# Optimization experiments

Hardware: AMD Instinct MI355X
Metric: run time of the kernel (lower is better)

Reference implementation:

```python
import jax, jax.numpy as jnp
import numpy as np

B, LQ, LK = 2, 2048, 77
DIM, XDIM = 320, 768
H, HD = 8, 40  # heads, head_dim; DIM == H*HD
FF = 4 * DIM  # GEGLU inner dim


def _ln(x, g, b, eps=1e-5):
    m = x.mean(-1, keepdims=True)
    v = ((x - m) ** 2).mean(-1, keepdims=True)
    return (x - m) * jax.lax.rsqrt(v + eps) * g + b


def _split_heads(x):  # [B,L,DIM] -> [B,H,L,HD]
    return x.reshape(x.shape[0], x.shape[1], H, HD).transpose(0, 2, 1, 3)


def _merge_heads(x):  # [B,H,L,HD] -> [B,L,DIM]
    return x.transpose(0, 2, 1, 3).reshape(x.shape[0], x.shape[2], H * HD)


def setup_inputs() -> dict:
    key = jax.random.key(0)
    ks = jax.random.split(key, 24)
    s = 0.02
    r = lambda i, shp: s * jax.random.normal(ks[i], shp, jnp.float32)
    return {
        "hidden_states": jax.random.normal(ks[0], (B, LQ, DIM), jnp.float32),
        "encoder_hidden_states": jax.random.normal(ks[1], (B, LK, XDIM), jnp.float32),
        # norm1 + self-attn (attn1)
        "ln1_g": jnp.ones((DIM,), jnp.float32), "ln1_b": jnp.zeros((DIM,), jnp.float32),
        "wq1": r(2, (DIM, DIM)), "wk1": r(3, (DIM, DIM)), "wv1": r(4, (DIM, DIM)),
        "wo1": r(5, (DIM, DIM)), "bo1": jnp.zeros((DIM,), jnp.float32),
        # norm2 + Hadamard cross-attn (attn2)
        "ln2_g": jnp.ones((DIM,), jnp.float32), "ln2_b": jnp.zeros((DIM,), jnp.float32),
        "wq2": r(6, (DIM, DIM)), "wk2": r(7, (XDIM, DIM)), "wvh": r(8, (DIM, DIM)),
        "wo2": r(9, (DIM, DIM)), "bo2": jnp.zeros((DIM,), jnp.float32),
        # norm3 + GEGLU feed-forward
        "ln3_g": jnp.ones((DIM,), jnp.float32), "ln3_b": jnp.zeros((DIM,), jnp.float32),
        "wff1": r(10, (DIM, 2 * FF)), "bff1": jnp.zeros((2 * FF,), jnp.float32),
        "wff2": r(11, (FF, DIM)), "bff2": jnp.zeros((DIM,), jnp.float32),
    }


def reference(hidden_states, encoder_hidden_states, ln1_g, ln1_b, wq1, wk1, wv1,
              wo1, bo1, ln2_g, ln2_b, wq2, wk2, wvh, wo2, bo2, ln3_g, ln3_b,
              wff1, bff1, wff2, bff2):
    scale = 1.0 / jnp.sqrt(jnp.asarray(HD, hidden_states.dtype))

    # ---- self-attention (SDPA semantics) ----
    h = _ln(hidden_states, ln1_g, ln1_b)
    q = _split_heads(h @ wq1)
    k = _split_heads(h @ wk1)
    v = _split_heads(h @ wv1)
    scores = jnp.einsum('bhqd,bhkd->bhqk', q, k) * scale
    w = jax.nn.softmax(scores, axis=-1)
    attn = jnp.einsum('bhqk,bhkd->bhqd', w, v)
    attn = _merge_heads(attn) @ wo1 + bo1
    hidden_states = hidden_states + attn

    # ---- Hadamard cross-attention: value comes from hidden_states (len Lq) ----
    h = _ln(hidden_states, ln2_g, ln2_b)
    q = _split_heads(h @ wq2)                     # [B,H,Lq,HD]
    k = _split_heads(encoder_hidden_states @ wk2) # [B,H,Lk,HD]
    vH = _split_heads(h @ wvh)                    # [B,H,Lq,HD]
    scores = jnp.einsum('bhqd,bhkd->bhqk', q, k) * scale
    w = jax.nn.softmax(scores, axis=-1)           # [B,H,Lq,Lk]
    # (w[...,None] * vH[...,None,:]).sum(-2) == vH * w.sum(-1, keepdims) (v indep of k)
    cross = vH * jnp.sum(w, axis=-1, keepdims=True)
    cross = _merge_heads(cross) @ wo2 + bo2
    hidden_states = hidden_states + cross

    # ---- GEGLU feed-forward ----
    h = _ln(hidden_states, ln3_g, ln3_b)
    proj = h @ wff1 + bff1
    x, gate = jnp.split(proj, 2, axis=-1)
    ff = (x * jax.nn.gelu(gate, approximate=False)) @ wff2 + bff2
    return hidden_states + ff
```

## Files before the change

kernel.cpp:

```cpp
#include <hip/hip_runtime.h>
#include <math.h>

#define DIM   320
#define HD    40
#define NH    8
#define LQ    2048
#define BATCH 2
#define MROWS 4096
#define FFD   1280
#define FF2   2560

#define KSPLIT 8
#define KCHUNK (LQ/KSPLIT)
#define KT     32
#define NT     (KCHUNK/KT)
#define NQROWS (BATCH*NH*LQ)

#define LSCALE (0.15811388300841897f * 1.4426950408889634f)

typedef unsigned short ushort_t;
typedef unsigned int u32;
using bf16x8 = __attribute__((ext_vector_type(8))) short;
using f32x4  = __attribute__((ext_vector_type(4))) float;

static __device__ inline ushort_t f2bf(float f) {
  union { float f; unsigned u; } x{f};
  unsigned r = x.u + 0x7FFFu + ((x.u >> 16) & 1u);
  return (ushort_t)(r >> 16);
}
static __device__ inline float bf2f(ushort_t h) {
  union { unsigned u; float f; } x; x.u = ((unsigned)h) << 16; return x.f;
}

__global__ __launch_bounds__(256) void ln_kernel(
    const float* __restrict__ X, const float* __restrict__ g,
    const float* __restrict__ bta, ushort_t* __restrict__ Y)
{
  int row  = blockIdx.x * 4 + (threadIdx.x >> 6);
  int lane = threadIdx.x & 63;
  const float* x = X + (size_t)row * DIM;
  float v[5];
  float s = 0.f;
#pragma unroll
  for (int i = 0; i < 5; ++i) { v[i] = x[lane + 64*i]; s += v[i]; }
#pragma unroll
  for (int off = 32; off >= 1; off >>= 1) s += __shfl_xor(s, off, 64);
  float mean = s * (1.0f/DIM);
  float sq = 0.f;
#pragma unroll
  for (int i = 0; i < 5; ++i) { float d = v[i] - mean; sq += d*d; }
#pragma unroll
  for (int off = 32; off >= 1; off >>= 1) sq += __shfl_xor(sq, off, 64);
  float rstd = rsqrtf(sq*(1.0f/DIM) + 1e-5f);
  ushort_t* y = Y + (size_t)row * DIM;
#pragma unroll
  for (int i = 0; i < 5; ++i) {
    int c = lane + 64*i;
    y[c] = f2bf((v[i]-mean)*rstd*g[c] + bta[c]);
  }
}

#define OFF_WQKVT 0
#define OFF_WO1T  (960*320)
#define OFF_WO2T  (OFF_WO1T + 320*320)
#define OFF_WFF1T (OFF_WO2T + 320*320)
#define OFF_WFF2T (OFF_WFF1T + 320*2560)
#define OFF_WVHB  (OFF_WFF2T + 1280*320)
#define WBF_TOTAL (OFF_WVHB + 320*320)

__global__ __launch_bounds__(256) void convw_kernel(
    const float* __restrict__ wq1, const float* __restrict__ wk1,
    const float* __restrict__ wv1, const float* __restrict__ wo1,
    const float* __restrict__ wo2, const float* __restrict__ wff1,
    const float* __restrict__ wff2, const float* __restrict__ wvh,
    ushort_t* __restrict__ dst, ushort_t* __restrict__ Kimg)
{
  int e = blockIdx.y;
  if (e == 8) {
    int f = blockIdx.x*256 + threadIdx.x;
    if (f < 98304) {
      int g3 = f/3, cidx = f - 3*g3;
      int rr = g3 & 31, tile = (g3 >> 5) & 63, bh = g3 >> 11;
      uint4 z = {0,0,0,0};
      *(uint4*)(Kimg + ((size_t)(bh*64 + tile))*2048 + rr*64
                + (((5+cidx) ^ (rr&7)) << 3)) = z;
    }
    return;
  }
  const float* src; int K, N; size_t doff; int tr = 1; float scale = 1.f;
  switch (e) {
    case 0: src=wq1;  K=320;  N=320;  doff=OFF_WQKVT; scale=LSCALE; break;
    case 1: src=wk1;  K=320;  N=320;  doff=OFF_WQKVT + 320*320;  break;
    case 2: src=wv1;  K=320;  N=320;  doff=OFF_WQKVT + 2*320*320;break;
    case 3: src=wo1;  K=320;  N=320;  doff=OFF_WO1T;             break;
    case 4: src=wo2;  K=320;  N=320;  doff=OFF_WO2T;             break;
    case 5: src=wff1; K=320;  N=2560; doff=OFF_WFF1T;            break;
    case 6: src=wff2; K=1280; N=320;  doff=OFF_WFF2T;            break;
    default: src=wvh; K=320;  N=320;  doff=OFF_WVHB; tr=0;       break;
  }
  int ntN = N/32;
  int nt_total = (K/32)*ntN;
  int t = blockIdx.x;
  if (t >= nt_total) return;
  int kt = t / ntN, nt = t - kt*ntN;
  __shared__ float tile[32][33];
  int tx = threadIdx.x & 31, ty = threadIdx.x >> 5;
  ushort_t* d = dst + doff;
#pragma unroll
  for (int i = 0; i < 4; ++i) {
    int r = ty + 8*i;
    tile[r][tx] = src[(size_t)(kt*32+r)*N + nt*32+tx] * scale;
  }
  __syncthreads();
  if (tr) {
#pragma unroll
    for (int i = 0; i < 4; ++i) {
      int r = ty + 8*i;
      d[(size_t)(nt*32+r)*K + kt*32+tx] = f2bf(tile[tx][r]);
    }
  } else {
#pragma unroll
    for (int i = 0; i < 4; ++i) {
      int r = ty + 8*i;
      d[(size_t)(kt*32+r)*N + nt*32+tx] = f2bf(tile[r][tx]);
    }
  }
}

#define AST 72
__global__ __launch_bounds__(256) void mgemm(
    const ushort_t* __restrict__ A, int lda,
    const ushort_t* __restrict__ Bt, int ldb,
    const float* __restrict__ bias,
    const float* __restrict__ R,
    float* __restrict__ Cf, ushort_t* __restrict__ Cb, int ldc,
    int K)
{
  __shared__ ushort_t As[64*AST];
  __shared__ ushort_t Bs[64*AST];
  int tid = threadIdx.x;
  int w = tid >> 6, lane = tid & 63, quad = lane >> 4, n16 = lane & 15;
  int wm = w >> 1, wn = w & 1;
  int bm = blockIdx.y * 64, bn = blockIdx.x * 64;
  int sr = tid >> 2, sc = (tid & 3) << 4;
  const ushort_t* Ag = A  + (size_t)(bm + sr)*lda + sc;
  const ushort_t* Bg = Bt + (size_t)(bn + sr)*ldb + sc;

  f32x4 acc00 = {0.f,0.f,0.f,0.f}, acc01 = acc00, acc10 = acc00, acc11 = acc00;

  float4 av0 = *(const float4*)(Ag);
  float4 av1 = *(const float4*)(Ag + 8);
  float4 bv0 = *(const float4*)(Bg);
  float4 bv1 = *(const float4*)(Bg + 8);
  for (int k0 = 0; k0 < K; k0 += 64) {
    __syncthreads();
    *(float4*)(As + sr*AST + sc)     = av0;
    *(float4*)(As + sr*AST + sc + 8) = av1;
    *(float4*)(Bs + sr*AST + sc)     = bv0;
    *(float4*)(Bs + sr*AST + sc + 8) = bv1;
    __syncthreads();
    if (k0 + 64 < K) {
      av0 = *(const float4*)(Ag + k0 + 64);
      av1 = *(const float4*)(Ag + k0 + 72);
      bv0 = *(const float4*)(Bg + k0 + 64);
      bv1 = *(const float4*)(Bg + k0 + 72);
    }
#pragma unroll
    for (int kk = 0; kk < 64; kk += 32) {
      bf16x8 fa0 = *(const bf16x8*)(As + (wm*32 +      n16)*AST + kk + quad*8);
      bf16x8 fa1 = *(const bf16x8*)(As + (wm*32 + 16 + n16)*AST + kk + quad*8);
      bf16x8 fb0 = *(const bf16x8*)(Bs + (wn*32 +      n16)*AST + kk + quad*8);
      bf16x8 fb1 = *(const bf16x8*)(Bs + (wn*32 + 16 + n16)*AST + kk + quad*8);
      acc00 = __builtin_amdgcn_mfma_f32_16x16x32_bf16(fa0, fb0, acc00, 0,0,0);
      acc01 = __builtin_amdgcn_mfma_f32_16x16x32_bf16(fa0, fb1, acc01, 0,0,0);
      acc10 = __builtin_amdgcn_mfma_f32_16x16x32_bf16(fa1, fb0, acc10, 0,0,0);
      acc11 = __builtin_amdgcn_mfma_f32_16x16x32_bf16(fa1, fb1, acc11, 0,0,0);
    }
  }

  f32x4 accs[2][2] = {{acc00, acc01},{acc10, acc11}};
#pragma unroll
  for (int s = 0; s < 2; ++s)
#pragma unroll
    for (int t = 0; t < 2; ++t) {
      int c = bn + wn*32 + t*16 + n16;
      float bb = bias ? bias[c] : 0.f;
#pragma unroll
      for (int i = 0; i < 4; ++i) {
        int r = bm + wm*32 + s*16 + quad*4 + i;
        float v = accs[s][t][i] + bb;
        if (R)  v += R[(size_t)r*ldc + c];
        if (Cf) Cf[(size_t)r*ldc + c] = v;
        if (Cb) Cb[(size_t)r*ldc + c] = f2bf(v);
      }
    }
}

#define AS_STRIDE 40
__global__ __launch_bounds__(256) void mgemm128_qkv(
    const ushort_t* __restrict__ A, const ushort_t* __restrict__ Bt,
    ushort_t* __restrict__ Qb, ushort_t* __restrict__ Kimg,
    ushort_t* __restrict__ Vimg)
{
  __shared__ ushort_t As[128*AST];
  __shared__ ushort_t Bs[64*AST];
  int tid = threadIdx.x;
  int w = tid >> 6, lane = tid & 63, quad = lane >> 4, n16 = lane & 15;
  int wm = w >> 1, wn = w & 1;
  int bm = blockIdx.y * 128, bn = blockIdx.x * 64;
  int ar = tid >> 2, ac = (tid & 3) << 4;
  const ushort_t* Ag0 = A  + (size_t)(bm + ar)*DIM + ac;
  const ushort_t* Ag1 = A  + (size_t)(bm + 64 + ar)*DIM + ac;
  const ushort_t* Bg  = Bt + (size_t)(bn + ar)*DIM + ac;

  f32x4 acc[4][2];
#pragma unroll
  for (int s = 0; s < 4; ++s)
#pragma unroll
    for (int t = 0; t < 2; ++t) acc[s][t] = f32x4{0.f,0.f,0.f,0.f};

  float4 a00 = *(const float4*)(Ag0);
  float4 a01 = *(const float4*)(Ag0 + 8);
  float4 a10 = *(const float4*)(Ag1);
  float4 a11 = *(const float4*)(Ag1 + 8);
  float4 b0  = *(const float4*)(Bg);
  float4 b1  = *(const float4*)(Bg + 8);
  for (int k0 = 0; k0 < DIM; k0 += 64) {
    __syncthreads();
    *(float4*)(As + ar*AST + ac)          = a00;
    *(float4*)(As + ar*AST + ac + 8)      = a01;
    *(float4*)(As + (64+ar)*AST + ac)     = a10;
    *(float4*)(As + (64+ar)*AST + ac + 8) = a11;
    *(float4*)(Bs + ar*AST + ac)          = b0;
    *(float4*)(Bs + ar*AST + ac + 8)      = b1;
    __syncthreads();
    if (k0 + 64 < DIM) {
      a00 = *(const float4*)(Ag0 + k0 + 64);
      a01 = *(const float4*)(Ag0 + k0 + 72);
      a10 = *(const float4*)(Ag1 + k0 + 64);
      a11 = *(const float4*)(Ag1 + k0 + 72);
      b0  = *(const float4*)(Bg  + k0 + 64);
      b1  = *(const float4*)(Bg  + k0 + 72);
    }
#pragma unroll
    for (int kk = 0; kk < 64; kk += 32) {
      bf16x8 fa[4], fb[2];
#pragma unroll
      for (int s = 0; s < 4; ++s)
        fa[s] = *(const bf16x8*)(As + (wm*64 + s*16 + n16)*AST + kk + quad*8);
#pragma unroll
      for (int t = 0; t < 2; ++t)
        fb[t] = *(const bf16x8*)(Bs + (wn*32 + t*16 + n16)*AST + kk + quad*8);
#pragma unroll
      for (int s = 0; s < 4; ++s)
#pragma unroll
        for (int t = 0; t < 2; ++t)
          acc[s][t] = __builtin_amdgcn_mfma_f32_16x16x32_bf16(fa[s], fb[t], acc[s][t], 0,0,0);
    }
  }

  int b8 = (bm >> 11) << 3;
  if (bn < 320) {
#pragma unroll
    for (int s = 0; s < 4; ++s)
#pragma unroll
      for (int t = 0; t < 2; ++t) {
        int c = bn + wn*32 + t*16 + n16;
#pragma unroll
        for (int i = 0; i < 4; ++i) {
          int r = bm + wm*64 + s*16 + quad*4 + i;
          Qb[(size_t)r*320 + c] = f2bf(acc[s][t][i]);
        }
      }
  } else if (bn < 640) {
#pragma unroll
    for (int t = 0; t < 2; ++t) {
      int c = bn + wn*32 + t*16 + n16 - 320;
      int hK = c / 40, d = c - hK*40;
#pragma unroll
      for (int s = 0; s < 4; ++s)
#pragma unroll
        for (int i = 0; i < 4; ++i) {
          int r = bm + wm*64 + s*16 + quad*4 + i;
          int l = r & 2047, tl = l >> 5, rr = l & 31;
          Kimg[((size_t)((b8 + hK)*64 + tl))*2048 + rr*64
               + (((d >> 3) ^ (rr & 7)) << 3) + (d & 7)] = f2bf(acc[s][t][i]);
        }
    }
  } else {
#pragma unroll
    for (int t = 0; t < 2; ++t) {
      int c = bn + wn*32 + t*16 + n16 - 640;
      int hV = c / 40, d = c - hV*40;
#pragma unroll
      for (int s = 0; s < 4; ++s) {
        int l0 = (bm + wm*64 + s*16 + quad*4) & 2047;
        int tl = l0 >> 5, p0 = (l0 & 31) >> 1;
        ushort_t* vb = Vimg + ((size_t)((b8 + hV)*64 + tl))*1536 + d*32;
#pragma unroll
        for (int j = 0; j < 2; ++j) {
          int p = p0 + j;
          unsigned val = (unsigned)f2bf(acc[s][t][2*j])
                       | ((unsigned)f2bf(acc[s][t][2*j+1]) << 16);
          *(unsigned*)(vb + (((p >> 2) ^ (d & 3)) << 3) + ((p & 3) << 1)) = val;
        }
      }
    }
  }
}

__global__ __launch_bounds__(256) void ff1_geglu(
    const ushort_t* __restrict__ A, const ushort_t* __restrict__ Bt,
    const float* __restrict__ bias, ushort_t* __restrict__ Og)
{
  __shared__ ushort_t As[128*AST];
  __shared__ ushort_t Bxs[64*AST];
  __shared__ ushort_t Bgs[64*AST];
  int tid = threadIdx.x;
  int w = tid >> 6, lane = tid & 63, quad = lane >> 4, n16 = lane & 15;
  int wm = w >> 1, wn = w & 1;
  int bm = blockIdx.y * 128, bn = blockIdx.x * 64;
  int ar = tid >> 2, ac = (tid & 3) << 4;
  const ushort_t* Ag0 = A  + (size_t)(bm + ar)*DIM + ac;
  const ushort_t* Ag1 = A  + (size_t)(bm + 64 + ar)*DIM + ac;
  const ushort_t* Bxg = Bt + (size_t)(bn + ar)*DIM + ac;
  const ushort_t* Bgg = Bt + (size_t)(bn + FFD + ar)*DIM + ac;

  f32x4 ax[4][2], ag[4][2];
#pragma unroll
  for (int s = 0; s < 4; ++s)
#pragma unroll
    for (int t = 0; t < 2; ++t) { ax[s][t] = f32x4{0.f,0.f,0.f,0.f}; ag[s][t] = ax[s][t]; }

  float4 a00 = *(const float4*)(Ag0);
  float4 a01 = *(const float4*)(Ag0 + 8);
  float4 a10 = *(const float4*)(Ag1);
  float4 a11 = *(const float4*)(Ag1 + 8);
  float4 bx0 = *(const float4*)(Bxg);
  float4 bx1 = *(const float4*)(Bxg + 8);
  float4 bg0 = *(const float4*)(Bgg);
  float4 bg1 = *(const float4*)(Bgg + 8);
  for (int k0 = 0; k0 < DIM; k0 += 64) {
    __syncthreads();
    *(float4*)(As  + ar*AST + ac)          = a00;
    *(float4*)(As  + ar*AST + ac + 8)      = a01;
    *(float4*)(As  + (64+ar)*AST + ac)     = a10;
    *(float4*)(As  + (64+ar)*AST + ac + 8) = a11;
    *(float4*)(Bxs + ar*AST + ac)          = bx0;
    *(float4*)(Bxs + ar*AST + ac + 8)      = bx1;
    *(float4*)(Bgs + ar*AST + ac)          = bg0;
    *(float4*)(Bgs + ar*AST + ac + 8)      = bg1;
    __syncthreads();
    if (k0 + 64 < DIM) {
      a00 = *(const float4*)(Ag0 + k0 + 64);
      a01 = *(const float4*)(Ag0 + k0 + 72);
      a10 = *(const float4*)(Ag1 + k0 + 64);
      a11 = *(const float4*)(Ag1 + k0 + 72);
      bx0 = *(const float4*)(Bxg + k0 + 64);
      bx1 = *(const float4*)(Bxg + k0 + 72);
      bg0 = *(const float4*)(Bgg + k0 + 64);
      bg1 = *(const float4*)(Bgg + k0 + 72);
    }
#pragma unroll
    for (int kk = 0; kk < 64; kk += 32) {
      bf16x8 fa[4], fx[2], fg[2];
#pragma unroll
      for (int s = 0; s < 4; ++s)
        fa[s] = *(const bf16x8*)(As + (wm*64 + s*16 + n16)*AST + kk + quad*8);
#pragma unroll
      for (int t = 0; t < 2; ++t) {
        fx[t] = *(const bf16x8*)(Bxs + (wn*32 + t*16 + n16)*AST + kk + quad*8);
        fg[t] = *(const bf16x8*)(Bgs + (wn*32 + t*16 + n16)*AST + kk + quad*8);
      }
#pragma unroll
      for (int s = 0; s < 4; ++s)
#pragma unroll
        for (int t = 0; t < 2; ++t) {
          ax[s][t] = __builtin_amdgcn_mfma_f32_16x16x32_bf16(fa[s], fx[t], ax[s][t], 0,0,0);
          ag[s][t] = __builtin_amdgcn_mfma_f32_16x16x32_bf16(fa[s], fg[t], ag[s][t], 0,0,0);
        }
    }
  }

  const float kk2 = 0.7071067811865476f;
#pragma unroll
  for (int s = 0; s < 4; ++s)
#pragma unroll
    for (int t = 0; t < 2; ++t) {
      int c = bn + wn*32 + t*16 + n16;
      float bx = bias[c], bg = bias[c + FFD];
#pragma unroll
      for (int i = 0; i < 4; ++i) {
        int r = bm + wm*64 + s*16 + quad*4 + i;
        float xx = ax[s][t][i] + bx;
        float gg = ag[s][t][i] + bg;
        Og[(size_t)r*FFD + c] = f2bf(xx * 0.5f * gg * (1.f + erff(gg * kk2)));
      }
    }
}

#define TILE_K_SH 2048
#define TILE_V_SH 1536
#define TILE_SH   (TILE_K_SH + TILE_V_SH)

__global__ __launch_bounds__(256, 2) void attn_mfma(
    const ushort_t* __restrict__ Qb, const ushort_t* __restrict__ Kimg,
    const ushort_t* __restrict__ Vimg,
    float* __restrict__ Pl, ushort_t* __restrict__ Pacc)
{
  __shared__ ushort_t lds[4*TILE_SH];
  int tid  = threadIdx.x;
  int w    = tid >> 6;
  int lane = tid & 63;
  int quad = lane >> 4;
  int n16  = lane & 15;

  int blk  = blockIdx.x;
  int bh   = (blk & 7) | (((blk >> 3) & 1) << 3);
  int rest = blk >> 4;
  int qt   = rest & 15;
  int ks   = rest >> 4;
  int b = bh >> 3, h = bh & 7;

  const ushort_t* qrowa = Qb + (size_t)(b*LQ + qt*128 + w*32 + n16)*320 + h*HD;
  const ushort_t* qrowb = qrowa + 16*320;
  bf16x8 qf0a = *(const bf16x8*)(qrowa + quad*8);
  bf16x8 qf1a = *(const bf16x8*)(qrowa + 32);
  bf16x8 qf0b = *(const bf16x8*)(qrowb + quad*8);
  bf16x8 qf1b = *(const bf16x8*)(qrowb + 32);

  const ushort_t* Ktb = Kimg + ((size_t)bh*64 + ks*NT)*TILE_K_SH;
  const ushort_t* Vtb = Vimg + ((size_t)bh*64 + ks*NT)*TILE_V_SH;

  int swk0 = (quad ^ (n16 & 7)) << 3;
  int swk1 = ((quad + 4) ^ (n16 & 7)) << 3;
  int kof0 = n16*64 + swk0;
  int kof1 = n16*64 + swk1;
  int kof2 = (16+n16)*64 + swk0;
  int kof3 = (16+n16)*64 + swk1;
  int swv  = (quad ^ (n16 & 3)) << 3;
  int vof0 = n16*32 + swv;
  int vof1 = (16+n16)*32 + swv;
  int vof2 = (32+n16)*32 + swv;

  f32x4 o0a = {0.f,0.f,0.f,0.f}, o1a = o0a, o2a = o0a;
  f32x4 o0b = o0a, o1b = o0a, o2b = o0a;
  f32x4 la0a = o0a, la1a = o0a, la0b = o0a, la1b = o0a;

#define CVTPK(D, LO, HI) \
  asm("v_cvt_pk_bf16_f32 %0, %1, %2" : "=v"(D) : "v"(LO), "v"(HI))
#define PSWAP32(X, Y) \
  asm("v_permlane32_swap_b32 %0, %1" : "+v"(X), "+v"(Y))
#define PSWAP16(X, Y) \
  asm("v_permlane16_swap_b32 %0, %1" : "+v"(X), "+v"(Y))

#define STAGE(SLOT, T) { \
  const ushort_t* ks_ = Ktb + (size_t)(T)*TILE_K_SH + w*512 + lane*8; \
  ushort_t* kd_ = lds + (SLOT)*TILE_SH + w*512; \
  __builtin_amdgcn_global_load_lds( \
      (const __attribute__((address_space(1))) u32*)ks_, \
      (__attribute__((address_space(3))) u32*)kd_, 16, 0, 0); \
  if (w < 3) { \
    const ushort_t* vs_ = Vtb + (size_t)(T)*TILE_V_SH + w*512 + lane*8; \
    ushort_t* vd_ = lds + (SLOT)*TILE_SH + TILE_K_SH + w*512; \
    __builtin_amdgcn_global_load_lds( \
        (const __attribute__((address_space(1))) u32*)vs_, \
        (__attribute__((address_space(3))) u32*)vd_, 16, 0, 0); \
  } }

#define HALF(Q0F, Q1F, LA0, LA1, FRAG) \
  bf16x8 FRAG; { \
  f32x4 st0 = {-8.f,-8.f,-8.f,-8.f}; f32x4 st1 = st0; \
  st0 = __builtin_amdgcn_mfma_f32_16x16x32_bf16(K00, Q0F, st0, 0,0,0); \
  st1 = __builtin_amdgcn_mfma_f32_16x16x32_bf16(K10, Q0F, st1, 0,0,0); \
  st0 = __builtin_amdgcn_mfma_f32_16x16x32_bf16(K01, Q1F, st0, 0,0,0); \
  st1 = __builtin_amdgcn_mfma_f32_16x16x32_bf16(K11, Q1F, st1, 0,0,0); \
  f32x4 p0, p1; \
  _Pragma("unroll") \
  for (int r = 0; r < 4; ++r) { p0[r] = exp2f(st0[r]); p1[r] = exp2f(st1[r]); } \
  LA0 += p0; LA1 += p1; \
  unsigned d0, d1, d2, d3; \
  CVTPK(d0, p0[0], p0[1]); CVTPK(d1, p0[2], p0[3]); \
  CVTPK(d2, p1[0], p1[1]); CVTPK(d3, p1[2], p1[3]); \
  PSWAP32(d0, d2); PSWAP16(d0, d2); \
  PSWAP32(d1, d3); PSWAP16(d1, d3); \
  union { unsigned u[4]; bf16x8 v; } fr_; \
  fr_.u[0] = d0; fr_.u[1] = d1; fr_.u[2] = d2; fr_.u[3] = d3; \
  FRAG = fr_.v; }

#define CTILE(SLOT) { \
  const ushort_t* Kb_ = lds + (SLOT)*TILE_SH; \
  const ushort_t* Vb_ = Kb_ + TILE_K_SH; \
  bf16x8 K00 = *(const bf16x8*)(Kb_ + kof0); \
  bf16x8 K01 = *(const bf16x8*)(Kb_ + kof1); \
  bf16x8 K10 = *(const bf16x8*)(Kb_ + kof2); \
  bf16x8 K11 = *(const bf16x8*)(Kb_ + kof3); \
  bf16x8 V0  = *(const bf16x8*)(Vb_ + vof0); \
  bf16x8 V1  = *(const bf16x8*)(Vb_ + vof1); \
  bf16x8 V2  = *(const bf16x8*)(Vb_ + vof2); \
  HALF(qf0a, qf1a, la0a, la1a, fragA) \
  HALF(qf0b, qf1b, la0b, la1b, fragB) \
  o0a = __builtin_amdgcn_mfma_f32_16x16x32_bf16(fragA, V0, o0a, 0,0,0); \
  o0b = __builtin_amdgcn_mfma_f32_16x16x32_bf16(fragB, V0, o0b, 0,0,0); \
  o1a = __builtin_amdgcn_mfma_f32_16x16x32_bf16(fragA, V1, o1a, 0,0,0); \
  o1b = __builtin_amdgcn_mfma_f32_16x16x32_bf16(fragB, V1, o1b, 0,0,0); \
  o2a = __builtin_amdgcn_mfma_f32_16x16x32_bf16(fragA, V2, o2a, 0,0,0); \
  o2b = __builtin_amdgcn_mfma_f32_16x16x32_bf16(fragB, V2, o2b, 0,0,0); }

  STAGE(0, 0); STAGE(1, 1);
  __syncthreads();
  for (int s = 0; s < NT/2; ++s) {
    int sb = s & 1;
    if (s + 1 < NT/2) {
      STAGE((sb^1)*2,     2*s + 2);
      STAGE((sb^1)*2 + 1, 2*s + 3);
    }
    CTILE(sb*2);
    CTILE(sb*2 + 1);
    __syncthreads();
  }
#undef STAGE
#undef CTILE
#undef HALF
#undef CVTPK
#undef PSWAP32
#undef PSWAP16

  float sA = la0a[0]+la0a[1]+la0a[2]+la0a[3] + la1a[0]+la1a[1]+la1a[2]+la1a[3];
  float sB = la0b[0]+la0b[1]+la0b[2]+la0b[3] + la1b[0]+la1b[1]+la1b[2]+la1b[3];
  sA += __shfl_xor(sA, 16, 64); sA += __shfl_xor(sA, 32, 64);
  sB += __shfl_xor(sB, 16, 64); sB += __shfl_xor(sB, 32, 64);

  int grow = bh*LQ + qt*128 + w*32;
  size_t base = (size_t)ks*NQROWS;
  if (lane < 16) {
    Pl[base + grow + n16]      = sA;
    Pl[base + grow + 16 + n16] = sB;
  }

  int gqa = grow + quad*4;
#pragma unroll
  for (int r = 0; r < 4; ++r) {
    size_t gq = base + gqa + r;
    ushort_t* pw = Pacc + gq*40;
    pw[n16]      = f2bf(o0a[r]);
    pw[16 + n16] = f2bf(o1a[r]);
    if (n16 < 8) pw[32 + n16] = f2bf(o2a[r]);
    size_t gq2 = gq + 16;
    ushort_t* pw2 = Pacc + gq2*40;
    pw2[n16]      = f2bf(o0b[r]);
    pw2[16 + n16] = f2bf(o1b[r]);
    if (n16 < 8) pw2[32 + n16] = f2bf(o2b[r]);
  }
}

__global__ __launch_bounds__(256) void attn_merge(
    const float* __restrict__ Pl, const ushort_t* __restrict__ Pacc,
    ushort_t* __restrict__ O)
{
  int t = blockIdx.x*256 + threadIdx.x;
  int idx = t / 5;
  int u   = t - idx*5;
  int bh = idx >> 11, qi = idx & (LQ-1);
  int b = bh >> 3, h = bh & 7;
  float L = 0.f;
#pragma unroll
  for (int k = 0; k < KSPLIT; ++k) L += Pl[(size_t)k*NQROWS + idx];
  float inv = 1.0f / L;
  float acc[8] = {0,0,0,0,0,0,0,0};
#pragma unroll
  for (int k = 0; k < KSPLIT; ++k) {
    const ushort_t* pr = Pacc + ((size_t)k*NQROWS + idx)*40 + u*8;
    ushort_t vbuf[8];
    *(uint4*)vbuf = *(const uint4*)pr;
#pragma unroll
    for (int j = 0; j < 8; ++j) acc[j] += bf2f(vbuf[j]);
  }
  ushort_t ob[8];
#pragma unroll
  for (int j = 0; j < 8; ++j) ob[j] = f2bf(acc[j]*inv);
  ushort_t* orow = O + (size_t)(b*LQ + qi)*DIM + h*HD;
  *(uint4*)(orow + u*8) = *(uint4*)ob;
}

extern "C" void kernel_launch(void* const* d_in, const int* in_sizes, int n_in,
                              void* d_out, int out_size, void* d_ws, size_t ws_size,
                              hipStream_t stream) {
  const float* hidden = (const float*)d_in[0];
  const float* ln1_g = (const float*)d_in[2];
  const float* ln1_b = (const float*)d_in[3];
  const float* wq1   = (const float*)d_in[4];
  const float* wk1   = (const float*)d_in[5];
  const float* wv1   = (const float*)d_in[6];
  const float* wo1   = (const float*)d_in[7];
  const float* bo1   = (const float*)d_in[8];
  const float* ln2_g = (const float*)d_in[9];
  const float* ln2_b = (const float*)d_in[10];
  const float* wvh   = (const float*)d_in[13];
  const float* wo2   = (const float*)d_in[14];
  const float* bo2   = (const float*)d_in[15];
  const float* ln3_g = (const float*)d_in[16];
  const float* ln3_b = (const float*)d_in[17];
  const float* wff1  = (const float*)d_in[18];
  const float* bff1  = (const float*)d_in[19];
  const float* wff2  = (const float*)d_in[20];
  const float* bff2  = (const float*)d_in[21];
  float* out = (float*)d_out;

  ushort_t* wsu = (ushort_t*)d_ws;
  ushort_t* wbf   = wsu;
  ushort_t* lnb   = wbf + WBF_TOTAL;
  ushort_t* Qb    = lnb + (size_t)MROWS*DIM;
  ushort_t* attnb = Qb + (size_t)MROWS*DIM;
  ushort_t* gegb  = attnb + (size_t)MROWS*DIM;
  ushort_t* wct   = gegb + (size_t)MROWS*FFD;
  ushort_t* vtb   = wct + 320*320;
  ushort_t* kpb   = vtb + (size_t)16*64*1536;
  ushort_t* Pacc  = kpb + (size_t)16*64*2048;
  float* fws = (float*)((((uintptr_t)(Pacc + (size_t)KSPLIT*NQROWS*40)) + 255) & ~(uintptr_t)255);
  float* h1   = fws;
  float* h2   = h1 + (size_t)MROWS*DIM;
  float* Pl   = h2 + (size_t)MROWS*DIM;

  dim3 t256(256);
  dim3 gconv(1024, 9);
  dim3 gqkv(15, 32);
  dim3 g320(5, 64);
  dim3 gwc(5, 5);
  dim3 gffg(20, 32);
  dim3 gattn(16*16*KSPLIT);

  convw_kernel<<<gconv, t256, 0, stream>>>(wq1, wk1, wv1, wo1, wo2, wff1, wff2,
                                           wvh, wbf, kpb);
  mgemm<<<gwc, t256, 0, stream>>>(wbf + OFF_WO2T, DIM, wbf + OFF_WVHB, DIM,
                                  nullptr, nullptr, nullptr, wct, DIM, DIM);

  ln_kernel<<<MROWS/4, t256, 0, stream>>>(hidden, ln1_g, ln1_b, lnb);
  mgemm128_qkv<<<gqkv, t256, 0, stream>>>(lnb, wbf + OFF_WQKVT, Qb, kpb, vtb);
  attn_mfma<<<gattn, t256, 0, stream>>>(Qb, kpb, vtb, Pl, Pacc);
  attn_merge<<<NQROWS*5/256, t256, 0, stream>>>(Pl, Pacc, attnb);
  mgemm<<<g320, t256, 0, stream>>>(attnb, DIM, wbf + OFF_WO1T, DIM, bo1, hidden,
                                   h1, nullptr, DIM, DIM);

  ln_kernel<<<MROWS/4, t256, 0, stream>>>(h1, ln2_g, ln2_b, lnb);
  mgemm<<<g320, t256, 0, stream>>>(lnb, DIM, wct, DIM, bo2, h1,
                                   h2, nullptr, DIM, DIM);

  ln_kernel<<<MROWS/4, t256, 0, stream>>>(h2, ln3_g, ln3_b, lnb);
  ff1_geglu<<<gffg, t256, 0, stream>>>(lnb, wbf + OFF_WFF1T, bff1, gegb);
  mgemm<<<g320, t256, 0, stream>>>(gegb, FFD, wbf + OFF_WFF2T, FFD, bff2, h2,
                                   out, nullptr, DIM, FFD);
}
```

Measured before the change: 211.4 us.

## Double-buffer generic GEMM with direct global-to-LDS loads and XOR swizzle

Rewrites the generic 64x64 bf16 MFMA GEMM to stage A/B tiles into LDS with global_load_lds and an XOR-swizzled layout instead of padded register-staged stores. Two LDS buffers allow the next K tile to load while the current one is consumed, removing one barrier per iteration and the register round-trip. LDS use doubles, and correctness depends on the async loads completing before the trailing barrier. The swizzle replaces the stride padding to avoid bank conflicts.

```diff
diff --git a/kernel.cpp b/kernel.cpp
--- a/kernel.cpp
+++ b/kernel.cpp
@@ -22,6 +22,9 @@
 typedef unsigned int u32;
 using bf16x8 = __attribute__((ext_vector_type(8))) short;
 using f32x4  = __attribute__((ext_vector_type(4))) float;
+
+#define AS1 __attribute__((address_space(1)))
+#define AS3 __attribute__((address_space(3)))
 
 static __device__ inline ushort_t f2bf(float f) {
   union { float f; unsigned u; } x{f};
@@ -127,7 +130,7 @@
   }
 }
 
-#define AST 72
+#define AS64 (64*64)
 __global__ __launch_bounds__(256) void mgemm(
     const ushort_t* __restrict__ A, int lda,
     const ushort_t* __restrict__ Bt, int ldb,
@@ -136,47 +139,63 @@
     float* __restrict__ Cf, ushort_t* __restrict__ Cb, int ldc,
     int K)
 {
-  __shared__ ushort_t As[64*AST];
-  __shared__ ushort_t Bs[64*AST];
+  __shared__ ushort_t As[2*AS64];
+  __shared__ ushort_t Bs[2*AS64];
   int tid = threadIdx.x;
   int w = tid >> 6, lane = tid & 63, quad = lane >> 4, n16 = lane & 15;
   int wm = w >> 1, wn = w & 1;
   int bm = blockIdx.y * 64, bn = blockIdx.x * 64;
-  int sr = tid >> 2, sc = (tid & 3) << 4;
-  const ushort_t* Ag = A  + (size_t)(bm + sr)*lda + sc;
-  const ushort_t* Bg = Bt + (size_t)(bn + sr)*ldb + sc;
+
+  int r0 = tid >> 3,        c0 = (tid & 7) ^ (r0 & 7);
+  int r1 = (tid+256) >> 3,  c1 = (tid & 7) ^ (r1 & 7);
+  const ushort_t* Ag0 = A  + (size_t)(bm + r0)*lda + c0*8;
+  const ushort_t* Ag1 = A  + (size_t)(bm + r1)*lda + c1*8;
+  const ushort_t* Bg0 = Bt + (size_t)(bn + r0)*ldb + c0*8;
+  const ushort_t* Bg1 = Bt + (size_t)(bn + r1)*ldb + c1*8;
+  int d0 = w*512, d1 = 2048 + w*512;
+
+#define STG(BUF, K0) { \
+  __builtin_amdgcn_global_load_lds((const AS1 u32*)(Ag0 + (K0)), \
+      (AS3 u32*)(As + (BUF)*AS64 + d0), 16, 0, 0); \
+  __builtin_amdgcn_global_load_lds((const AS1 u32*)(Ag1 + (K0)), \
+      (AS3 u32*)(As + (BUF)*AS64 + d1), 16, 0, 0); \
+  __builtin_amdgcn_global_load_lds((const AS1 u32*)(Bg0 + (K0)), \
+      (AS3 u32*)(Bs + (BUF)*AS64 + d0), 16, 0, 0); \
+  __builtin_amdgcn_global_load_lds((const AS1 u32*)(Bg1 + (K0)), \
+      (AS3 u32*)(Bs + (BUF)*AS64 + d1), 16, 0, 0); }
+
+  int sw0 = ( quad      ^ (n16 & 7)) << 3;
+  int sw1 = ((quad + 4) ^ (n16 & 7)) << 3;
+  int aof0 = (wm*32 +      n16)*64;
+  int aof1 = (wm*32 + 16 + n16)*64;
+  int bof0 = (wn*32 +      n16)*64;
+  int bof1 = (wn*32 + 16 + n16)*64;
 
   f32x4 acc00 = {0.f,0.f,0.f,0.f}, acc01 = acc00, acc10 = acc00, acc11 = acc00;
 
-  float4 av0 = *(const float4*)(Ag);
-  float4 av1 = *(const float4*)(Ag + 8);
-  float4 bv0 = *(const float4*)(Bg);
-  float4 bv1 = *(const float4*)(Bg + 8);
+  STG(0, 0);
+  __syncthreads();
+  int buf = 0;
   for (int k0 = 0; k0 < K; k0 += 64) {
-    __syncthreads();
-    *(float4*)(As + sr*AST + sc)     = av0;
-    *(float4*)(As + sr*AST + sc + 8) = av1;
-    *(float4*)(Bs + sr*AST + sc)     = bv0;
-    *(float4*)(Bs + sr*AST + sc + 8) = bv1;
-    __syncthreads();
-    if (k0 + 64 < K) {
-      av0 = *(const float4*)(Ag + k0 + 64);
-      av1 = *(const float4*)(Ag + k0 + 72);
-      bv0 = *(const float4*)(Bg + k0 + 64);
-      bv1 = *(const float4*)(Bg + k0 + 72);
-    }
-#pragma unroll
-    for (int kk = 0; kk < 64; kk += 32) {
-      bf16x8 fa0 = *(const bf16x8*)(As + (wm*32 +      n16)*AST + kk + quad*8);
-      bf16x8 fa1 = *(const bf16x8*)(As + (wm*32 + 16 + n16)*AST + kk + quad*8);
-      bf16x8 fb0 = *(const bf16x8*)(Bs + (wn*32 +      n16)*AST + kk + quad*8);
-      bf16x8 fb1 = *(const bf16x8*)(Bs + (wn*32 + 16 + n16)*AST + kk + quad*8);
+    if (k0 + 64 < K) STG(buf^1, k0 + 64);
+    const ushort_t* Ab = As + buf*AS64;
+    const ushort_t* Bb = Bs + buf*AS64;
+#pragma unroll
+    for (int kk = 0; kk < 2; ++kk) {
+      int sw = kk ? sw1 : sw0;
+      bf16x8 fa0 = *(const bf16x8*)(Ab + aof0 + sw);
+      bf16x8 fa1 = *(const bf16x8*)(Ab + aof1 + sw);
+      bf16x8 fb0 = *(const bf16x8*)(Bb + bof0 + sw);
+      bf16x8 fb1 = *(const bf16x8*)(Bb + bof1 + sw);
       acc00 = __builtin_amdgcn_mfma_f32_16x16x32_bf16(fa0, fb0, acc00, 0,0,0);
       acc01 = __builtin_amdgcn_mfma_f32_16x16x32_bf16(fa0, fb1, acc01, 0,0,0);
       acc10 = __builtin_amdgcn_mfma_f32_16x16x32_bf16(fa1, fb0, acc10, 0,0,0);
       acc11 = __builtin_amdgcn_mfma_f32_16x16x32_bf16(fa1, fb1, acc11, 0,0,0);
     }
-  }
+    __syncthreads();
+    buf ^= 1;
+  }
+#undef STG
 
   f32x4 accs[2][2] = {{acc00, acc01},{acc10, acc11}};
 #pragma unroll
@@ -196,7 +215,7 @@
     }
 }
 
-#define AS_STRIDE 40
+#define AST 72
 __global__ __launch_bounds__(256) void mgemm128_qkv(
     const ushort_t* __restrict__ A, const ushort_t* __restrict__ Bt,
     ushort_t* __restrict__ Qb, ushort_t* __restrict__ Kimg,
@@ -458,14 +477,12 @@
   const ushort_t* ks_ = Ktb + (size_t)(T)*TILE_K_SH + w*512 + lane*8; \
   ushort_t* kd_ = lds + (SLOT)*TILE_SH + w*512; \
   __builtin_amdgcn_global_load_lds( \
-      (const __attribute__((address_space(1))) u32*)ks_, \
-      (__attribute__((address_space(3))) u32*)kd_, 16, 0, 0); \
+      (const AS1 u32*)ks_, (AS3 u32*)kd_, 16, 0, 0); \
   if (w < 3) { \
     const ushort_t* vs_ = Vtb + (size_t)(T)*TILE_V_SH + w*512 + lane*8; \
     ushort_t* vd_ = lds + (SLOT)*TILE_SH + TILE_K_SH + w*512; \
     __builtin_amdgcn_global_load_lds( \
-        (const __attribute__((address_space(1))) u32*)vs_, \
-        (__attribute__((address_space(3))) u32*)vd_, 16, 0, 0); \
+        (const AS1 u32*)vs_, (AS3 u32*)vd_, 16, 0, 0); \
   } }
 
 #define HALF(Q0F, Q1F, LA0, LA1, FRAG) \
```

Result: no change. 215.6 us (+2.0%).
